# Kernel optimization log

Measured on AMD Instinct MI355X. Metric: run time of the kernel, lower is better.

The kernel has to match this reference:

```python
import jax, jax.numpy as jnp
import numpy as np

N, IN, H, M, D = 2048, 400, 256, 128, 8


def setup_inputs() -> dict:
    key = jax.random.key(0)
    ks = jax.random.split(key, 20)
    g = lambda k, shp, s: jax.random.normal(k, shp, jnp.float32) * s
    C = IN // 2
    return {
        "x": g(ks[0], (N, IN), 1.0),
        "memory": g(ks[1], (N, H, M), 1.0),
        "ke_w": g(ks[2], (H, C), 1.0 / np.sqrt(C)),
        "ke_b": g(ks[3], (H,), 0.01),
        "km_w": g(ks[4], (M, H), 1.0 / np.sqrt(H)),
        "km_b": g(ks[5], (M,), 0.01),
        "kw2_w": g(ks[6], (D, H), 1.0 / np.sqrt(H)),
        "kw2_b": g(ks[7], (D,), 0.01),
        "sum_w": g(ks[8], (H, 2 * H), 1.0 / np.sqrt(2 * H)),
        "sum_b": g(ks[9], (H,), 0.01),
        "out_w": g(ks[10], (1, H), 1.0 / np.sqrt(H)),
        "out_b": g(ks[11], (1,), 0.01),
        "ve_w": g(ks[12], (H, IN), 1.0 / np.sqrt(IN)),
        "ve_b": g(ks[13], (H,), 0.01),
        "er_w": g(ks[14], (D, H, H), 1.0 / np.sqrt(H)),
        "er_b": g(ks[15], (D, H), 0.01),
        "ad_w": g(ks[16], (D, H, H), 1.0 / np.sqrt(H)),
        "ad_b": g(ks[17], (D, H), 0.01),
    }


def reference(x, memory, ke_w, ke_b, km_w, km_b, kw2_w, kw2_b,
              sum_w, sum_b, out_w, out_b, ve_w, ve_b,
              er_w, er_b, ad_w, ad_b):
    n, c2 = x.shape
    c = c2 // 2
    # query = sum of the two halves of x
    q = x.reshape(n, 2, c).sum(axis=1)                       # (N, C)
    k = q @ ke_w.T + ke_b                                    # (N, H)
    w = jax.nn.softmax(k @ km_w.T + km_b, axis=-1)           # (N, M) read/write weights
    w2 = jax.nn.softmax(k @ kw2_w.T + kw2_b, axis=-1)        # (N, D) expert gates
    # memory read: weighted sum over memory slots
    r = jnp.einsum('nhm,nm->nh', memory, w)                  # (N, H)
    f = jnp.tanh(jnp.concatenate([k, r], axis=1) @ sum_w.T + sum_b)
    y = f @ out_w.T + out_b                                  # (N, 1)
    v = x @ ve_w.T + ve_b                                    # (N, H)
    # DynamicLinear: gate-weighted mixture of per-expert linear maps
    # (fused: avoids materializing per-sample (N,H,H) weights)
    e = jax.nn.sigmoid(jnp.einsum('ni,doi,nd->no', v, er_w, w2) + w2 @ er_b)
    a = jnp.tanh(jnp.einsum('ni,doi,nd->no', v, ad_w, w2) + w2 @ ad_b)
    # memory write: erase then add
    memory = memory * (1.0 - w[:, None, :] * e[:, :, None])
    memory = memory + w[:, None, :] * a[:, :, None]
    return y, memory
```

## Files before the change

### kernel.cpp

```cpp
#include <hip/hip_runtime.h>
#include <math.h>

#define N_  2048
#define IN_ 400
#define C_  200
#define H_  256
#define M_  128
#define D_  8

#define KQ   224
#define KX   416
#define KBIG 2112
#define NZ   6
#define KSPL (KBIG / NZ)
#define KS   512

typedef __bf16 bf16x8 __attribute__((ext_vector_type(8)));
typedef float  f32x4  __attribute__((ext_vector_type(4)));

__device__ __forceinline__ ushort f2bf(float x) { __bf16 b = (__bf16)x; return __builtin_bit_cast(ushort, b); }
__device__ __forceinline__ float  bf2f(ushort u) { unsigned v = ((unsigned)u) << 16; return __builtin_bit_cast(float, v); }

__device__ __forceinline__ float4 f4z() { return make_float4(0.f, 0.f, 0.f, 0.f); }
__device__ __forceinline__ float4 ld4p(const float* p, bool v) { return v ? *(const float4*)p : f4z(); }
__device__ __forceinline__ float4 add4(float4 a, float4 b) {
    return make_float4(a.x + b.x, a.y + b.y, a.z + b.z, a.w + b.w);
}
__device__ __forceinline__ uint4 pack8(float4 a, float4 b) {
    ushort u[8] = { f2bf(a.x), f2bf(a.y), f2bf(a.z), f2bf(a.w),
                    f2bf(b.x), f2bf(b.y), f2bf(b.z), f2bf(b.w) };
    return *(uint4*)u;
}

template<class F>
__device__ __forceinline__ void gemm_core(
    F&& ld, const float* __restrict__ bias,
    void* __restrict__ Cv, int ldc, int outbf,
    int m0, int n0, int kFrom, int kTo,
    ushort (*As)[128][40], ushort (*Bs)[64][40])
{
    const int tid = threadIdx.x, lane = tid & 63, wave = tid >> 6;
    const int wm = (wave >> 1) * 64, wn = (wave & 1) * 32;
    const int sr = tid >> 2, sc = (tid & 3) * 8;

    f32x4 acc[4][2] = {};

    auto compute = [&](int b) {
        const int ko = (lane >> 4) * 8;
        bf16x8 af[4], bfr[2];
#pragma unroll
        for (int i = 0; i < 4; i++)
            af[i] = __builtin_bit_cast(bf16x8, *(const uint4*)&As[b][wm + i * 16 + (lane & 15)][ko]);
#pragma unroll
        for (int j = 0; j < 2; j++)
            bfr[j] = __builtin_bit_cast(bf16x8, *(const uint4*)&Bs[b][wn + j * 16 + (lane & 15)][ko]);
#pragma unroll
        for (int i = 0; i < 4; i++)
#pragma unroll
            for (int j = 0; j < 2; j++)
                acc[i][j] = __builtin_amdgcn_mfma_f32_16x16x32_bf16(af[i], bfr[j], acc[i][j], 0, 0, 0);
    };

    uint4 a0, a1, b0;
    ld(kFrom, a0, a1, b0);
    *(uint4*)&As[0][sr][sc] = a0;
    *(uint4*)&As[0][sr + 64][sc] = a1;
    *(uint4*)&Bs[0][sr][sc] = b0;
    __syncthreads();

    int cur = 0;
    for (int k0 = kFrom + 32; k0 < kTo; k0 += 32) {
        ld(k0, a0, a1, b0);
        compute(cur);
        *(uint4*)&As[cur ^ 1][sr][sc] = a0;
        *(uint4*)&As[cur ^ 1][sr + 64][sc] = a1;
        *(uint4*)&Bs[cur ^ 1][sr][sc] = b0;
        __syncthreads();
        cur ^= 1;
    }
    compute(cur);

    float* Cf = (float*)Cv;
    ushort* Cb = (ushort*)Cv;
#pragma unroll
    for (int i = 0; i < 4; i++) {
#pragma unroll
        for (int j = 0; j < 2; j++) {
            int row = m0 + wm + i * 16 + (lane >> 4) * 4;
            int col = n0 + wn + j * 16 + (lane & 15);
#pragma unroll
            for (int r = 0; r < 4; r++) {
                float val = acc[i][j][r];
                if (bias) val += bias[col];
                if (outbf) Cb[(size_t)(row + r) * ldc + col] = f2bf(val);
                else       Cf[(size_t)(row + r) * ldc + col] = val;
            }
        }
    }
}

__global__ __launch_bounds__(256) void k1_kernel(
    const float* __restrict__ x,
    const float* __restrict__ ke_w, const float* __restrict__ ke_b, ushort* __restrict__ kr,
    const float* __restrict__ ve_w, const float* __restrict__ ve_b, float* __restrict__ v,
    const float* __restrict__ er_w, const float* __restrict__ er_b,
    const float* __restrict__ ad_w, const float* __restrict__ ad_b,
    ushort* __restrict__ wcat)
{
    __shared__ ushort As[2][128][40];
    __shared__ ushort Bs[2][64][40];
    const int z = blockIdx.z;
    const int sr = threadIdx.x >> 2, sc = (threadIdx.x & 3) * 8;

    if (z == 0) {
        const int m0 = blockIdx.y * 128, n0 = blockIdx.x * 64;
        auto ld = [&](int k0, uint4& A0, uint4& A1, uint4& B0) {
            int c0 = k0 + sc, c4 = c0 + 4;
            bool v0 = c0 < C_, v4 = c4 < C_;
            const float* r0 = x + (size_t)(m0 + sr) * IN_;
            const float* r1 = x + (size_t)(m0 + sr + 64) * IN_;
            A0 = pack8(add4(ld4p(r0 + c0, v0), ld4p(r0 + C_ + c0, v0)),
                       add4(ld4p(r0 + c4, v4), ld4p(r0 + C_ + c4, v4)));
            A1 = pack8(add4(ld4p(r1 + c0, v0), ld4p(r1 + C_ + c0, v0)),
                       add4(ld4p(r1 + c4, v4), ld4p(r1 + C_ + c4, v4)));
            const float* rb = ke_w + (size_t)(n0 + sr) * C_;
            B0 = pack8(ld4p(rb + c0, v0), ld4p(rb + c4, v4));
        };
        gemm_core(ld, ke_b, kr, KS, 1, m0, n0, 0, KQ, As, Bs);
    } else if (z == 1) {
        const int m0 = blockIdx.y * 128, n0 = blockIdx.x * 64;
        auto ld = [&](int k0, uint4& A0, uint4& A1, uint4& B0) {
            int c0 = k0 + sc, c4 = c0 + 4;
            bool v0 = c0 < IN_, v4 = c4 < IN_;
            const float* r0 = x + (size_t)(m0 + sr) * IN_;
            const float* r1 = x + (size_t)(m0 + sr + 64) * IN_;
            A0 = pack8(ld4p(r0 + c0, v0), ld4p(r0 + c4, v4));
            A1 = pack8(ld4p(r1 + c0, v0), ld4p(r1 + c4, v4));
            const float* rb = ve_w + (size_t)(n0 + sr) * IN_;
            B0 = pack8(ld4p(rb + c0, v0), ld4p(rb + c4, v4));
        };
        gemm_core(ld, ve_b, v, H_, 0, m0, n0, 0, KX, As, Bs);
    } else {
        int idx = ((z - 2) * 64 + blockIdx.y * 4 + blockIdx.x) * 256 + threadIdx.x;
        if (idx >= 512 * (KBIG / 4)) return;
        int oc = idx / (KBIG / 4), g = idx % (KBIG / 4), c0 = g * 4;
        const float* Wsrc = (oc < 256) ? er_w : ad_w;
        const float* bsrc = (oc < 256) ? er_b : ad_b;
        int oo = oc & 255;
        ushort pk[4];
#pragma unroll
        for (int j = 0; j < 4; j++) {
            int c = c0 + j;
            float val = 0.f;
            if (c < 2048)      { int d = c >> 8, ii = c & 255; val = Wsrc[(size_t)(d * 256 + oo) * 256 + ii]; }
            else if (c < 2056) { val = bsrc[(c - 2048) * 256 + oo]; }
            pk[j] = f2bf(val);
        }
        *(ushort4*)&wcat[(size_t)oc * KBIG + c0] = *(ushort4*)pk;
    }
}

__global__ __launch_bounds__(256) void vww_kernel(
    const ushort* __restrict__ kr, const float* __restrict__ v,
    const float* __restrict__ kw2_w, const float* __restrict__ kw2_b,
    const float* __restrict__ km_w, const float* __restrict__ km_b,
    float* __restrict__ wlog, ushort* __restrict__ vw)
{
    __shared__ ushort As[2][128][40];
    __shared__ ushort Bs[2][64][40];
    __shared__ float kf[H_], vl[H_], lg[8], w2l[8];
    const int b = blockIdx.x, t = threadIdx.x;
    const int sr = t >> 2, sc = (t & 3) * 8;

    if (b < 32) {
        const int m0 = (b >> 1) * 128, n0 = (b & 1) * 64;
        auto ld = [&](int k0, uint4& A0, uint4& A1, uint4& B0) {
            A0 = *(const uint4*)&kr[(size_t)(m0 + sr) * KS + k0 + sc];
            A1 = *(const uint4*)&kr[(size_t)(m0 + sr + 64) * KS + k0 + sc];
            int c0 = k0 + sc, c4 = c0 + 4;
            const float* rb = km_w + (size_t)(n0 + sr) * H_;
            B0 = pack8(*(const float4*)(rb + c0), *(const float4*)(rb + c4));
        };
        gemm_core(ld, km_b, wlog, M_, 0, m0, n0, 0, H_, As, Bs);
        return;
    }

    const int n = b - 32;
    if (t < 64) {
        ushort4 u = ((const ushort4*)(kr + (size_t)n * KS))[t];
        kf[t * 4 + 0] = bf2f(u.x); kf[t * 4 + 1] = bf2f(u.y);
        kf[t * 4 + 2] = bf2f(u.z); kf[t * 4 + 3] = bf2f(u.w);
        float4 vv = ((const float4*)(v + (size_t)n * H_))[t];
        vl[t * 4 + 0] = vv.x; vl[t * 4 + 1] = vv.y;
        vl[t * 4 + 2] = vv.z; vl[t * 4 + 3] = vv.w;
    }
    __syncthreads();
    {
        int d = t >> 5, l = t & 31;
        float acc = 0.f;
        const float* wr = kw2_w + d * H_;
#pragma unroll
        for (int s = 0; s < 8; s++) acc += kf[l + 32 * s] * wr[l + 32 * s];
#pragma unroll
        for (int off = 16; off; off >>= 1) acc += __shfl_xor(acc, off);
        if (l == 0) lg[d] = acc + kw2_b[d];
    }
    __syncthreads();
    if (t < 8) {
        float val = lg[t];
        float mx = val;
#pragma unroll
        for (int off = 1; off < 8; off <<= 1) mx = fmaxf(mx, __shfl_xor(mx, off));
        float e = expf(val - mx), s = e;
#pragma unroll
        for (int off = 1; off < 8; off <<= 1) s += __shfl_xor(s, off);
        w2l[t] = e / s;
    }
    __syncthreads();
    ushort* row = vw + (size_t)n * KBIG;
    for (int g = t; g < KBIG / 4; g += 256) {
        int c0 = g * 4;
        ushort pk[4];
#pragma unroll
        for (int j = 0; j < 4; j++) {
            int c = c0 + j;
            float val = 0.f;
            if (c < 2048)      val = w2l[c >> 8] * vl[c & 255];
            else if (c < 2056) val = w2l[c - 2048];
            pk[j] = f2bf(val);
        }
        *(ushort4*)&row[c0] = *(ushort4*)pk;
    }
}

__global__ __launch_bounds__(256) void bigw_kernel(
    const ushort* __restrict__ vw, const ushort* __restrict__ Wcat,
    float* __restrict__ parts)
{
    __shared__ ushort As[2][128][40];
    __shared__ ushort Bs[2][64][40];
    const int z = blockIdx.z;
    const int m0 = blockIdx.y * 128, n0 = blockIdx.x * 64;
    const int sr = threadIdx.x >> 2, sc = (threadIdx.x & 3) * 8;
    auto ld = [&](int k0, uint4& A0, uint4& A1, uint4& B0) {
        A0 = *(const uint4*)&vw[(size_t)(m0 + sr) * KBIG + k0 + sc];
        A1 = *(const uint4*)&vw[(size_t)(m0 + sr + 64) * KBIG + k0 + sc];
        B0 = *(const uint4*)&Wcat[(size_t)(n0 + sr) * KBIG + k0 + sc];
    };
    gemm_core(ld, nullptr, parts + (size_t)z * N_ * 512, 512, 0,
              m0, n0, z * KSPL, (z + 1) * KSPL, As, Bs);
}

__global__ __launch_bounds__(256) void mem_stream_kernel(
    const float* __restrict__ mem_in,
    const float* __restrict__ wlog,
    const float* __restrict__ parts,
    float* __restrict__ mem_out,
    ushort* __restrict__ kr)
{
    __shared__ float wl[M_];
    __shared__ float el[128], al[128];
    __shared__ float red[4];
    const int n = blockIdx.x >> 1, half = blockIdx.x & 1, hbase = half * 128;
    const int t = threadIdx.x;

    const int col = (t < 128) ? (hbase + t) : (256 + hbase + (t - 128));
    float pacc = 0.f;
#pragma unroll
    for (int z = 0; z < NZ; z++)
        pacc += parts[(size_t)z * N_ * 512 + (size_t)n * 512 + col];

    float lv = 0.f;
    if (t < 128) {
        lv = wlog[(size_t)n * M_ + t];
        float mx = lv;
#pragma unroll
        for (int off = 32; off; off >>= 1) mx = fmaxf(mx, __shfl_xor(mx, off));
        if ((t & 63) == 0) red[t >> 6] = mx;
        el[t] = 1.f / (1.f + expf(-pacc));
    } else {
        al[t - 128] = tanhf(pacc);
    }
    __syncthreads();
    if (t < 128) {
        float gmax = fmaxf(red[0], red[1]);
        float ev = expf(lv - gmax);
        float s = ev;
#pragma unroll
        for (int off = 32; off; off >>= 1) s += __shfl_xor(s, off);
        if ((t & 63) == 0) red[2 + (t >> 6)] = s;
        wl[t] = ev;
    }
    __syncthreads();
    if (t < 128) wl[t] *= 1.f / (red[2] + red[3]);
    __syncthreads();

    const int wave = t >> 6, lane = t & 63, half2 = lane >> 5, l32 = lane & 31;
    const f32x4* min4 = (const f32x4*)(mem_in + ((size_t)n * H_ + hbase) * M_);
    f32x4* mout4 = (f32x4*)(mem_out + ((size_t)n * H_ + hbase) * M_);
    f32x4 wv = ((const f32x4*)wl)[l32];
#pragma unroll 4
    for (int i = 0; i < 16; i++) {
        int hl = i * 8 + wave * 2 + half2;
        f32x4 mv = min4[hl * 32 + l32];
        float eh = el[hl], ah = al[hl];
        f32x4 nv = mv * (1.f - wv * eh) + wv * ah;
        __builtin_nontemporal_store(nv, &mout4[hl * 32 + l32]);
        float racc = mv[0] * wv[0] + mv[1] * wv[1] + mv[2] * wv[2] + mv[3] * wv[3];
#pragma unroll
        for (int off = 1; off < 32; off <<= 1) racc += __shfl_xor(racc, off);
        if (l32 == 0) kr[(size_t)n * KS + H_ + hbase + hl] = f2bf(racc);
    }
}

__global__ __launch_bounds__(256) void fy_kernel(
    const ushort* __restrict__ kr, const float* __restrict__ sum_w,
    const float* __restrict__ sum_b, const float* __restrict__ out_w,
    const float* __restrict__ out_b, float* __restrict__ y)
{
    __shared__ ushort As[2][64][40];
    __shared__ ushort Bs[2][256][40];
    __shared__ float yl[64][4];
    const int tid = threadIdx.x, lane = tid & 63, wave = tid >> 6;
    const int wn = wave * 64;
    const int m0 = blockIdx.x * 64;
    const int sr = tid >> 2, sc = (tid & 3) * 8;

    f32x4 acc[4][4] = {};

    auto compute = [&](int b) {
        const int ko = (lane >> 4) * 8;
        bf16x8 af[4], bfr[4];
#pragma unroll
        for (int i = 0; i < 4; i++)
            af[i] = __builtin_bit_cast(bf16x8, *(const uint4*)&As[b][i * 16 + (lane & 15)][ko]);
#pragma unroll
        for (int j = 0; j < 4; j++)
            bfr[j] = __builtin_bit_cast(bf16x8, *(const uint4*)&Bs[b][wn + j * 16 + (lane & 15)][ko]);
#pragma unroll
        for (int i = 0; i < 4; i++)
#pragma unroll
            for (int j = 0; j < 4; j++)
                acc[i][j] = __builtin_amdgcn_mfma_f32_16x16x32_bf16(af[i], bfr[j], acc[i][j], 0, 0, 0);
    };

    auto stage = [&](int buf, int k0) {
        int c0 = k0 + sc, c4 = c0 + 4;
        *(uint4*)&As[buf][sr][sc] = *(const uint4*)&kr[(size_t)(m0 + sr) * KS + k0 + sc];
#pragma unroll
        for (int g = 0; g < 4; g++) {
            const float* rb = sum_w + (size_t)(sr + g * 64) * KS;
            *(uint4*)&Bs[buf][sr + g * 64][sc] = pack8(*(const float4*)(rb + c0), *(const float4*)(rb + c4));
        }
    };

    stage(0, 0);
    __syncthreads();
    int cur = 0;
    for (int k0 = 32; k0 < KS; k0 += 32) {
        compute(cur);
        stage(cur ^ 1, k0);
        __syncthreads();
        cur ^= 1;
    }
    compute(cur);

    float ow[4], sb[4];
#pragma unroll
    for (int j = 0; j < 4; j++) {
        int col = wn + j * 16 + (lane & 15);
        ow[j] = out_w[col];
        sb[j] = sum_b[col];
    }
    float yp[4][4];
#pragma unroll
    for (int i = 0; i < 4; i++)
#pragma unroll
        for (int r = 0; r < 4; r++) {
            float s = 0.f;
#pragma unroll
            for (int j = 0; j < 4; j++)
                s += tanhf(acc[i][j][r] + sb[j]) * ow[j];
            yp[i][r] = s;
        }
#pragma unroll
    for (int off = 1; off < 16; off <<= 1)
#pragma unroll
        for (int i = 0; i < 4; i++)
#pragma unroll
            for (int r = 0; r < 4; r++)
                yp[i][r] += __shfl_xor(yp[i][r], off);
    if ((lane & 15) == 0) {
#pragma unroll
        for (int i = 0; i < 4; i++)
#pragma unroll
            for (int r = 0; r < 4; r++)
                yl[i * 16 + (lane >> 4) * 4 + r][wave] = yp[i][r];
    }
    __syncthreads();
    if (tid < 64)
        y[m0 + tid] = yl[tid][0] + yl[tid][1] + yl[tid][2] + yl[tid][3] + out_b[0];
}

extern "C" void kernel_launch(void* const* d_in, const int* in_sizes, int n_in,
                              void* d_out, int out_size, void* d_ws, size_t ws_size,
                              hipStream_t stream) {
    const float* x      = (const float*)d_in[0];
    const float* mem_in = (const float*)d_in[1];
    const float* ke_w   = (const float*)d_in[2];
    const float* ke_b   = (const float*)d_in[3];
    const float* km_w   = (const float*)d_in[4];
    const float* km_b   = (const float*)d_in[5];
    const float* kw2_w  = (const float*)d_in[6];
    const float* kw2_b  = (const float*)d_in[7];
    const float* sum_w  = (const float*)d_in[8];
    const float* sum_b  = (const float*)d_in[9];
    const float* out_w  = (const float*)d_in[10];
    const float* out_b  = (const float*)d_in[11];
    const float* ve_w   = (const float*)d_in[12];
    const float* ve_b   = (const float*)d_in[13];
    const float* er_w   = (const float*)d_in[14];
    const float* er_b   = (const float*)d_in[15];
    const float* ad_w   = (const float*)d_in[16];
    const float* ad_b   = (const float*)d_in[17];

    float* y_out   = (float*)d_out;
    float* mem_out = (float*)d_out + N_;

    float* ws = (float*)d_ws;
    size_t o = 0;
    float*  parts = ws + o;            o += (size_t)NZ * N_ * 512;
    ushort* vw    = (ushort*)(ws + o); o += (size_t)N_ * KBIG / 2;
    ushort* Wcat  = (ushort*)(ws + o); o += (size_t)512 * KBIG / 2;
    ushort* kr    = (ushort*)(ws + o); o += (size_t)N_ * KS / 2;
    float*  v     = ws + o;            o += (size_t)N_ * H_;
    float*  wlog  = ws + o;            o += (size_t)N_ * M_;

    k1_kernel<<<dim3(4, 16, 19), 256, 0, stream>>>(
        x, ke_w, ke_b, kr, ve_w, ve_b, v, er_w, er_b, ad_w, ad_b, Wcat);
    vww_kernel<<<32 + N_, 256, 0, stream>>>(
        kr, v, kw2_w, kw2_b, km_w, km_b, wlog, vw);
    bigw_kernel<<<dim3(8, 16, NZ), 256, 0, stream>>>(vw, Wcat, parts);
    mem_stream_kernel<<<2 * N_, 256, 0, stream>>>(mem_in, wlog, parts, mem_out, kr);
    fy_kernel<<<N_ / 64, 256, 0, stream>>>(kr, sum_w, sum_b, out_w, out_b, y_out);
}
```

Before: 177.0 us.

## Split memory update into gate-prep kernel and flat elementwise streaming kernel

```diff
diff --git a/kernel.cpp b/kernel.cpp
--- a/kernel.cpp
+++ b/kernel.cpp
@@ -251,24 +251,21 @@
               m0, n0, z * KSPL, (z + 1) * KSPL, As, Bs);
 }
 
-__global__ __launch_bounds__(256) void mem_stream_kernel(
-    const float* __restrict__ mem_in,
-    const float* __restrict__ wlog,
-    const float* __restrict__ parts,
-    float* __restrict__ mem_out,
-    ushort* __restrict__ kr)
-{
-    __shared__ float wl[M_];
-    __shared__ float el[128], al[128];
+__global__ __launch_bounds__(256) void eaw_kernel(
+    const float* __restrict__ wlog, const float* __restrict__ parts,
+    float* __restrict__ wbuf, float* __restrict__ ebuf, float* __restrict__ abuf)
+{
     __shared__ float red[4];
-    const int n = blockIdx.x >> 1, half = blockIdx.x & 1, hbase = half * 128;
-    const int t = threadIdx.x;
-
-    const int col = (t < 128) ? (hbase + t) : (256 + hbase + (t - 128));
-    float pacc = 0.f;
-#pragma unroll
-    for (int z = 0; z < NZ; z++)
-        pacc += parts[(size_t)z * N_ * 512 + (size_t)n * 512 + col];
+    const int n = blockIdx.x, t = threadIdx.x;
+
+    float s0 = 0.f, s1 = 0.f;
+#pragma unroll
+    for (int z = 0; z < NZ; z++) {
+        s0 += parts[(size_t)z * N_ * 512 + (size_t)n * 512 + t];
+        s1 += parts[(size_t)z * N_ * 512 + (size_t)n * 512 + 256 + t];
+    }
+    ebuf[(size_t)n * H_ + t] = 1.f / (1.f + expf(-s0));
+    abuf[(size_t)n * H_ + t] = tanhf(s1);
 
     float lv = 0.f;
     if (t < 128) {
@@ -277,9 +274,6 @@
 #pragma unroll
         for (int off = 32; off; off >>= 1) mx = fmaxf(mx, __shfl_xor(mx, off));
         if ((t & 63) == 0) red[t >> 6] = mx;
-        el[t] = 1.f / (1.f + expf(-pacc));
-    } else {
-        al[t - 128] = tanhf(pacc);
     }
     __syncthreads();
     if (t < 128) {
@@ -289,28 +283,33 @@
 #pragma unroll
         for (int off = 32; off; off >>= 1) s += __shfl_xor(s, off);
         if ((t & 63) == 0) red[2 + (t >> 6)] = s;
-        wl[t] = ev;
-    }
-    __syncthreads();
-    if (t < 128) wl[t] *= 1.f / (red[2] + red[3]);
-    __syncthreads();
-
-    const int wave = t >> 6, lane = t & 63, half2 = lane >> 5, l32 = lane & 31;
-    const f32x4* min4 = (const f32x4*)(mem_in + ((size_t)n * H_ + hbase) * M_);
-    f32x4* mout4 = (f32x4*)(mem_out + ((size_t)n * H_ + hbase) * M_);
-    f32x4 wv = ((const f32x4*)wl)[l32];
-#pragma unroll 4
-    for (int i = 0; i < 16; i++) {
-        int hl = i * 8 + wave * 2 + half2;
-        f32x4 mv = min4[hl * 32 + l32];
-        float eh = el[hl], ah = al[hl];
-        f32x4 nv = mv * (1.f - wv * eh) + wv * ah;
-        __builtin_nontemporal_store(nv, &mout4[hl * 32 + l32]);
-        float racc = mv[0] * wv[0] + mv[1] * wv[1] + mv[2] * wv[2] + mv[3] * wv[3];
-#pragma unroll
-        for (int off = 1; off < 32; off <<= 1) racc += __shfl_xor(racc, off);
-        if (l32 == 0) kr[(size_t)n * KS + H_ + hbase + hl] = f2bf(racc);
-    }
+        __syncthreads();
+        wbuf[(size_t)n * M_ + t] = ev / (red[2] + red[3]);
+    }
+}
+
+__global__ __launch_bounds__(256) void mem_stream_kernel(
+    const float* __restrict__ mem_in,
+    const float* __restrict__ wbuf, const float* __restrict__ ebuf,
+    const float* __restrict__ abuf,
+    float* __restrict__ mem_out, ushort* __restrict__ kr)
+{
+    const int idx = blockIdx.x * 256 + threadIdx.x;
+    const int n = idx >> 13, h = (idx >> 5) & 255, m4 = idx & 31;
+
+    f32x4 mv = ((const f32x4*)mem_in)[idx];
+    f32x4 wv = ((const f32x4*)wbuf)[(n << 5) + m4];
+    float eh = ebuf[(n << 8) + h];
+    float ah = abuf[(n << 8) + h];
+
+    f32x4 nv = mv * (1.f - wv * eh) + wv * ah;
+    ((f32x4*)mem_out)[idx] = nv;
+
+    float r = mv[0] * wv[0] + mv[1] * wv[1] + mv[2] * wv[2] + mv[3] * wv[3];
+#pragma unroll
+    for (int off = 1; off < 32; off <<= 1) r += __shfl_xor(r, off);
+    if ((threadIdx.x & 31) == 0)
+        kr[(size_t)n * KS + H_ + h] = f2bf(r);
 }
 
 __global__ __launch_bounds__(256) void fy_kernel(
@@ -435,12 +434,17 @@
     ushort* kr    = (ushort*)(ws + o); o += (size_t)N_ * KS / 2;
     float*  v     = ws + o;            o += (size_t)N_ * H_;
     float*  wlog  = ws + o;            o += (size_t)N_ * M_;
+    float*  wbuf  = ws + o;            o += (size_t)N_ * M_;
+    float*  ebuf  = ws + o;            o += (size_t)N_ * H_;
+    float*  abuf  = ws + o;            o += (size_t)N_ * H_;
 
     k1_kernel<<<dim3(4, 16, 19), 256, 0, stream>>>(
         x, ke_w, ke_b, kr, ve_w, ve_b, v, er_w, er_b, ad_w, ad_b, Wcat);
     vww_kernel<<<32 + N_, 256, 0, stream>>>(
         kr, v, kw2_w, kw2_b, km_w, km_b, wlog, vw);
     bigw_kernel<<<dim3(8, 16, NZ), 256, 0, stream>>>(vw, Wcat, parts);
-    mem_stream_kernel<<<2 * N_, 256, 0, stream>>>(mem_in, wlog, parts, mem_out, kr);
+    eaw_kernel<<<N_, 256, 0, stream>>>(wlog, parts, wbuf, ebuf, abuf);
+    mem_stream_kernel<<<(N_ * H_ * M_ / 4) / 256, 256, 0, stream>>>(
+        mem_in, wbuf, ebuf, abuf, mem_out, kr);
     fy_kernel<<<N_ / 64, 256, 0, stream>>>(kr, sum_w, sum_b, out_w, out_b, y_out);
 }
```

Measured after the change: 182.7 us. 1.03x slower.
